# Kernel tuning notes

Measured on AMD Instinct MI355X. Metric: run time of the kernel, lower is better.

## Reference

```python
import jax, jax.numpy as jnp
import numpy as np

B, C, L, D, P = 64, 64, 720, 512, 336
P2, H = P // 2, 512  # H = hidden width of the ProbG branch


def setup_inputs() -> dict:
    key = jax.random.key(0)
    ks = jax.random.split(key, 20)
    def w(k, i, o):
        return jax.random.normal(k, (i, o), jnp.float32) / np.sqrt(i)
    return {
        "x_bsd": jax.random.normal(ks[0], (B, L, C), jnp.float32),
        "z0": jax.random.normal(ks[1], (B, C, D), jnp.float32),
        "y0": jax.random.normal(ks[2], (B, C, P), jnp.float32),
        # ProbG hidden branch (HID_GIVEN_X_V0 -> SS_Z_GIVEN_X_V0)
        "W_h": w(ks[3], L, H),
        "W_ssz": w(ks[4], H, 2 * D),
        # x->z scale/shift flows (versions v2..v5)
        "W_xz_v2": w(ks[5], L, 2 * D),
        "W_xz_v3": w(ks[6], L, 2 * D),
        "W_xz_v4": w(ks[7], L, 2 * D),
        "W_xz_v5": w(ks[8], L, 2 * D),
        # z->x scale/shift flows (v0, v2, v3, v5)
        "W_zx_v0": w(ks[9], D, 2 * L),
        "W_zx_v2": w(ks[10], D, 2 * L),
        "W_zx_v3": w(ks[11], D, 2 * L),
        "W_zx_v5": w(ks[12], D, 2 * L),
        # z->y scale/shift flow (v4, used inside encoding)
        "W_zy_v4": w(ks[13], D, 2 * P),
        # decode heads: ROT_IN_Y_V1 and KOO_Y_GIVEN_Z_V0
        "W_rot": w(ks[14], D, P2),
        "W_koo": w(ks[15], D, 2 * P),
        # Koopman complex params for y-space (a + i b per channel/pair)
        "a_y": jnp.ones((C, P2), jnp.float32),
        "b_y": jnp.zeros((C, P2), jnp.float32) + 0.1,
    }


def _ss(params):
    """Split conditioner output into (positive scale, shift)."""
    s_raw, t = jnp.split(params, 2, axis=-1)
    return jnp.exp(jnp.tanh(s_raw)), t


def _affine(v, cond, W):
    """Scale/shift flow: v <- v * s(cond) + t(cond)."""
    s, t = _ss(jnp.einsum('bck,km->bcm', cond, W))
    return v * s + t


def _rot(u, theta, inv=False):
    """Rotate interleaved (re, im) pairs of u [B,C,P] by angles theta [B,C,P/2]."""
    re, im = u[..., 0::2], u[..., 1::2]
    th = -theta if inv else theta
    c, s = jnp.cos(th), jnp.sin(th)
    return jnp.stack([c * re - s * im, s * re + c * im], axis=-1).reshape(u.shape)


def _koop(u, a, b, inv=False):
    """Koopman unit-complex multiply on interleaved pairs; a,b [C,P/2]."""
    n = jnp.sqrt(a * a + b * b)
    ca, cb = a / n, b / n
    cb = -cb if inv else cb
    re, im = u[..., 0::2], u[..., 1::2]
    return jnp.stack([ca * re - cb * im, cb * re + ca * im], axis=-1).reshape(u.shape)


def reference(x_bsd, z0, y0, W_h, W_ssz, W_xz_v2, W_xz_v3, W_xz_v4, W_xz_v5,
              W_zx_v0, W_zx_v2, W_zx_v3, W_zx_v5, W_zy_v4, W_rot, W_koo, a_y, b_y):
    x = jnp.transpose(x_bsd, (0, 2, 1))  # [B,C,L]
    z = z0 * 0.1                          # [B,C,D]
    y = y0 * 0.1                          # [B,C,P]
    # ---- encoding phase ----
    h = jax.nn.gelu(jnp.einsum('bcl,lk->bck', x, W_h))  # X_to_Z_PROB hidden
    z = _affine(z, h, W_ssz)
    x = _affine(x, z, W_zx_v0)
    z = _affine(z, x, W_xz_v2); x = _affine(x, z, W_zx_v2)
    z = _affine(z, x, W_xz_v3); x = _affine(x, z, W_zx_v3)
    z = _affine(z, x, W_xz_v4); y = _affine(y, z, W_zy_v4)  # Z_to_Y_V4
    z = _affine(z, x, W_xz_v5); x = _affine(x, z, W_zx_v5)
    pre_y = y
    # ---- decode: rotate -> ky -> scale -> ky.inv -> rot.inv -> shift ----
    theta = jnp.pi * jnp.tanh(jnp.einsum('bcd,dp->bcp', z, W_rot))   # [B,C,P/2]
    scale, shift = _ss(jnp.einsum('bcd,dp->bcp', z, W_koo))          # [B,C,P]
    const = _koop(_rot(pre_y, theta), a_y, b_y)
    accu = const * scale
    accu = _rot(_koop(accu, a_y, b_y, inv=True), theta, inv=True) + shift
    return jnp.transpose(accu, (0, 2, 1))  # [B,P,C]
```

## Files before the change

kernel.cpp:

```cpp
#include <hip/hip_runtime.h>
#include <hip/hip_bf16.h>
#include <math.h>

#define BB  64
#define CC  64
#define LL  720
#define LLP 736
#define DD  512
#define PP  336
#define P2C 168
#define HH  512
#define MM  (BB*CC)

typedef _Float16 f16x8 __attribute__((ext_vector_type(8)));
typedef float    f32x4 __attribute__((ext_vector_type(4)));

#define GLDS16(g, l) __builtin_amdgcn_global_load_lds( \
    (const __attribute__((address_space(1))) void*)(g), \
    (__attribute__((address_space(3))) void*)(l), 16, 0, 0)

struct WDesc { const float* src; _Float16* dstHi; _Float16* dstLo;
               int K, N, Kpad, tbase, tilesN; };
struct WTab  { WDesc d[12]; };

__global__ __launch_bounds__(256) void k_convert(WTab tab) {
  __shared__ float tile[16][17];
  const int bid = blockIdx.x;
  int wi = 0;
#pragma unroll
  for (int i = 1; i < 12; ++i) if (bid >= tab.d[i].tbase) wi = i;
  const WDesc d = tab.d[wi];
  const int lt = bid - d.tbase;
  const int tk = lt / d.tilesN, tn = lt % d.tilesN;
  const int k0 = tk * 16, n0 = tn * 16;
  const int tx = threadIdx.x & 15, ty = threadIdx.x >> 4;
  float v = 0.f;
  if (n0 + tx < d.N) v = d.src[(size_t)(k0 + ty) * d.N + n0 + tx];
  tile[ty][tx] = v;
  __syncthreads();
  if (n0 + ty < d.N) {
    const float w = tile[tx][ty];
    const _Float16 h = (_Float16)w;
    const _Float16 l = (_Float16)(w - (float)h);
    const size_t base = (size_t)(n0 + ty) * d.Kpad;
    d.dstHi[base + k0 + tx] = h;
    d.dstLo[base + k0 + tx] = l;
    if (d.Kpad != d.K && k0 + 16 == d.K) {
      d.dstHi[base + d.K + tx] = (_Float16)0.f;
      d.dstLo[base + d.K + tx] = (_Float16)0.f;
    }
  }
}

__global__ __launch_bounds__(256) void k_xpose(const float* __restrict__ xbsd,
                                               _Float16* __restrict__ xhi,
                                               _Float16* __restrict__ xlo) {
  __shared__ float tile[16][17];
  const int b = blockIdx.z, l0 = blockIdx.x * 16, c0 = blockIdx.y * 16;
  const int tx = threadIdx.x, ty = threadIdx.y;
  tile[ty][tx] = xbsd[(size_t)b * LL * CC + (size_t)(l0 + ty) * CC + c0 + tx];
  __syncthreads();
  const float v = tile[tx][ty];
  const _Float16 h = (_Float16)v;
  const _Float16 l = (_Float16)(v - (float)h);
  const size_t m = (size_t)b * CC + c0 + ty;
  xhi[m * LLP + l0 + tx] = h;
  xlo[m * LLP + l0 + tx] = l;
  if (l0 == 704) {
    xhi[m * LLP + 720 + tx] = (_Float16)0.f;
    xlo[m * LLP + 720 + tx] = (_Float16)0.f;
  }
}

template<int EPI, bool DUAL, bool VIN16, bool OUT_T>
__global__ __launch_bounds__(256)
void k_gemm(const _Float16* Ahi, const _Float16* Alo, int lda,
            const _Float16* Whi, const _Float16* Wlo, int ldw,
            const float* Vin32, const _Float16* VinHi,
            const _Float16* VinLo, int ldv, float vscale,
            float* outT32,
            _Float16* outHi, _Float16* outLo, int ldo,
            int Kp, int Nv) {
  constexpr int NB   = DUAL ? 128 : 64;
  constexpr int ABUF = 64 * 32;
  constexpr int BBUF = NB * 32;
  constexpr int SBUF = 2 * ABUF + 2 * BBUF;
  constexpr int NCH  = 8 + 2 * (NB / 16);
  constexpr int NCHW = NCH / 4;
  __shared__ _Float16 smem[2 * SBUF];

  const int m0 = blockIdx.y * 64;
  const int n0 = blockIdx.x * 64;
  const int tid = threadIdx.x;
  const int w = tid >> 6, lane = tid & 63, q = lane >> 4, r = lane & 15;
  const int wr = (w & 1) * 32, wc = (w >> 1) * 32;
  const int lr = lane >> 2, ls = lane & 3;

  f32x4 accS[2][2] = {};
  f32x4 accT[2][2] = {};

  auto stage = [&](int kc, int bsel) {
    const int k0 = kc << 5;
    _Float16* sb = smem + bsel * SBUF;
#pragma unroll
    for (int cc = 0; cc < NCHW; ++cc) {
      const int chunk = w * NCHW + cc;
      const _Float16* gsrc;
      _Float16* ldst;
      if (chunk < 4) {
        const int rb = chunk * 16;
        const int R = rb + lr;
        const int ss = ls ^ ((R >> 1) & 3);
        gsrc = Ahi + (size_t)(m0 + R) * lda + k0 + ss * 8;
        ldst = sb + rb * 32;
      } else if (chunk < 8) {
        const int rb = (chunk - 4) * 16;
        const int R = rb + lr;
        const int ss = ls ^ ((R >> 1) & 3);
        gsrc = Alo + (size_t)(m0 + R) * lda + k0 + ss * 8;
        ldst = sb + ABUF + rb * 32;
      } else if (chunk < 8 + NB / 16) {
        const int rb = (chunk - 8) * 16;
        const int R = rb + lr;
        const int ss = ls ^ ((R >> 1) & 3);
        const int wrow = (R < 64) ? (n0 + R) : (Nv + n0 + (R - 64));
        gsrc = Whi + (size_t)wrow * ldw + k0 + ss * 8;
        ldst = sb + 2 * ABUF + rb * 32;
      } else {
        const int rb = (chunk - 8 - NB / 16) * 16;
        const int R = rb + lr;
        const int ss = ls ^ ((R >> 1) & 3);
        const int wrow = (R < 64) ? (n0 + R) : (Nv + n0 + (R - 64));
        gsrc = Wlo + (size_t)wrow * ldw + k0 + ss * 8;
        ldst = sb + 2 * ABUF + BBUF + rb * 32;
      }
      GLDS16(gsrc, ldst);
    }
  };

  const int nk = Kp >> 5;
  stage(0, 0);
  int cur = 0;
  for (int kc = 0; kc < nk; ++kc) {
    __syncthreads();
    if (kc + 1 < nk) stage(kc + 1, cur ^ 1);
    const _Float16* sb = smem + cur * SBUF;

    f16x8 ah[2], al[2];
#pragma unroll
    for (int rt = 0; rt < 2; ++rt) {
      const int R = wr + rt * 16 + r;
      const int t = (q ^ ((R >> 1) & 3)) * 8;
      ah[rt] = *(const f16x8*)(sb + R * 32 + t);
      al[rt] = *(const f16x8*)(sb + ABUF + R * 32 + t);
    }
#pragma unroll
    for (int ct = 0; ct < 2; ++ct) {
      const int RB = wc + ct * 16 + r;
      const int tb = (q ^ ((RB >> 1) & 3)) * 8;
      const f16x8 bh = *(const f16x8*)(sb + 2 * ABUF + RB * 32 + tb);
      const f16x8 bl = *(const f16x8*)(sb + 2 * ABUF + BBUF + RB * 32 + tb);
#pragma unroll
      for (int rt = 0; rt < 2; ++rt) {
        accS[rt][ct] = __builtin_amdgcn_mfma_f32_16x16x32_f16(ah[rt], bh, accS[rt][ct], 0, 0, 0);
        accS[rt][ct] = __builtin_amdgcn_mfma_f32_16x16x32_f16(al[rt], bh, accS[rt][ct], 0, 0, 0);
        accS[rt][ct] = __builtin_amdgcn_mfma_f32_16x16x32_f16(ah[rt], bl, accS[rt][ct], 0, 0, 0);
      }
      if (DUAL) {
        const int RT = 64 + RB;
        const int tt = (q ^ ((RT >> 1) & 3)) * 8;
        const f16x8 chh = *(const f16x8*)(sb + 2 * ABUF + RT * 32 + tt);
        const f16x8 cll = *(const f16x8*)(sb + 2 * ABUF + BBUF + RT * 32 + tt);
#pragma unroll
        for (int rt = 0; rt < 2; ++rt) {
          accT[rt][ct] = __builtin_amdgcn_mfma_f32_16x16x32_f16(ah[rt], chh, accT[rt][ct], 0, 0, 0);
          accT[rt][ct] = __builtin_amdgcn_mfma_f32_16x16x32_f16(al[rt], chh, accT[rt][ct], 0, 0, 0);
          accT[rt][ct] = __builtin_amdgcn_mfma_f32_16x16x32_f16(ah[rt], cll, accT[rt][ct], 0, 0, 0);
        }
      }
    }
    cur ^= 1;
  }

#pragma unroll
  for (int rt = 0; rt < 2; ++rt) {
    const int mb = m0 + wr + rt * 16 + q * 4;
#pragma unroll
    for (int ct = 0; ct < 2; ++ct) {
      const int n = n0 + wc + ct * 16 + r;
      if (n >= Nv) continue;
      if (EPI == 2) {
        *(f32x4*)(outT32 + (size_t)n * MM + mb) = accS[rt][ct];
      } else if (EPI == 1) {
#pragma unroll
        for (int g = 0; g < 4; ++g) {
          const int m = mb + g;
          const float v = accS[rt][ct][g];
          const float o = 0.5f * v * (1.0f + tanhf(0.7978845608028654f * (v + 0.044715f * v * v * v)));
          const _Float16 h = (_Float16)o;
          outHi[(size_t)m * ldo + n] = h;
          outLo[(size_t)m * ldo + n] = (_Float16)(o - (float)h);
        }
      } else {
        f32x4 o;
#pragma unroll
        for (int g = 0; g < 4; ++g) {
          const int m = mb + g;
          float v;
          if (VIN16) {
            v = (float)VinHi[(size_t)m * ldv + n] + (float)VinLo[(size_t)m * ldv + n];
          } else {
            v = Vin32[(size_t)m * ldv + n];
          }
          const float s = expf(tanhf(accS[rt][ct][g]));
          o[g] = v * vscale * s + accT[rt][ct][g];
        }
        if (OUT_T) {
          *(f32x4*)(outT32 + (size_t)n * MM + mb) = o;
        } else {
#pragma unroll
          for (int g = 0; g < 4; ++g) {
            const int m = mb + g;
            const _Float16 h = (_Float16)o[g];
            outHi[(size_t)m * ldo + n] = h;
            outLo[(size_t)m * ldo + n] = (_Float16)(o[g] - (float)h);
          }
        }
      }
    }
  }
}

__global__ __launch_bounds__(256) void k_final(const float* __restrict__ Pt,
                                               const float* __restrict__ yT,
                                               const float* __restrict__ Ay,
                                               const float* __restrict__ By,
                                               float* __restrict__ out) {
  const int c = threadIdx.x;
  const int j = blockIdx.x * 4 + threadIdx.y;
  const int b = blockIdx.y;
  const int m = b * 64 + c;
  const float th = 3.14159265358979323846f * tanhf(Pt[(size_t)j * MM + m]);
  const float sc0 = expf(tanhf(Pt[(size_t)(168 + 2 * j) * MM + m]));
  const float sc1 = expf(tanhf(Pt[(size_t)(169 + 2 * j) * MM + m]));
  const float t0 = Pt[(size_t)(504 + 2 * j) * MM + m];
  const float t1 = Pt[(size_t)(505 + 2 * j) * MM + m];
  const float re = yT[(size_t)(2 * j) * MM + m];
  const float im = yT[(size_t)(2 * j + 1) * MM + m];
  const float a = Ay[c * P2C + j], bb = By[c * P2C + j];
  const float rn = rsqrtf(a * a + bb * bb);
  const float ca = a * rn, cb = bb * rn;
  float s1v, c1;
  sincosf(th, &s1v, &c1);
  const float r1 = c1 * re - s1v * im, i1 = s1v * re + c1 * im;
  const float r2 = ca * r1 - cb * i1,  i2 = cb * r1 + ca * i1;
  const float r3 = r2 * sc0,           i3 = i2 * sc1;
  const float r4 = ca * r3 + cb * i3,  i4 = ca * i3 - cb * r3;
  const float r5 = c1 * r4 + s1v * i4, i5 = c1 * i4 - s1v * r4;
  out[(size_t)b * PP * CC + (size_t)(2 * j) * CC + c]     = r5 + t0;
  out[(size_t)b * PP * CC + (size_t)(2 * j + 1) * CC + c] = i5 + t1;
}

extern "C" void kernel_launch(void* const* d_in, const int* in_sizes, int n_in,
                              void* d_out, int out_size, void* d_ws, size_t ws_size,
                              hipStream_t stream) {
  const float* x_bsd   = (const float*)d_in[0];
  const float* z0      = (const float*)d_in[1];
  const float* y0      = (const float*)d_in[2];
  const float* W_h     = (const float*)d_in[3];
  const float* W_ssz   = (const float*)d_in[4];
  const float* W_xz_v2 = (const float*)d_in[5];
  const float* W_xz_v3 = (const float*)d_in[6];
  const float* W_xz_v4 = (const float*)d_in[7];
  const float* W_xz_v5 = (const float*)d_in[8];
  const float* W_zx_v0 = (const float*)d_in[9];
  const float* W_zx_v2 = (const float*)d_in[10];
  const float* W_zx_v3 = (const float*)d_in[11];
  const float* W_zy_v4 = (const float*)d_in[13];
  const float* W_rot   = (const float*)d_in[14];
  const float* W_koo   = (const float*)d_in[15];
  const float* a_y     = (const float*)d_in[16];
  const float* b_y     = (const float*)d_in[17];
  float* out = (float*)d_out;

  char* p = (char*)d_ws;
  auto alloc = [&](size_t bytes) -> void* {
    void* r = (void*)p; p += (bytes + 255) & ~(size_t)255; return r;
  };
  float*    yT  = (float*)alloc((size_t)PP * MM * 4);
  float*    Pt  = (float*)alloc((size_t)(P2C * 5) * MM * 4);
  _Float16* xhi = (_Float16*)alloc((size_t)MM * LLP * 2);
  _Float16* xlo = (_Float16*)alloc((size_t)MM * LLP * 2);
  _Float16* zhi = (_Float16*)alloc((size_t)MM * DD * 2);
  _Float16* zlo = (_Float16*)alloc((size_t)MM * DD * 2);
  _Float16* hhi = (_Float16*)alloc((size_t)MM * HH * 2);
  _Float16* hlo = (_Float16*)alloc((size_t)MM * HH * 2);
  auto wpair = [&](size_t elems, _Float16** lo) -> _Float16* {
    _Float16* hi = (_Float16*)alloc(elems * 2);
    *lo = (_Float16*)alloc(elems * 2);
    return hi;
  };
  _Float16 *tWhL, *tWsszL, *tWxz2L, *tWxz3L, *tWxz4L, *tWxz5L;
  _Float16 *tWzx0L, *tWzx2L, *tWzx3L, *tWzyL, *tWcatL;
  _Float16* tWh   = wpair((size_t)HH * LLP, &tWhL);
  _Float16* tWssz = wpair((size_t)(2*DD) * DD, &tWsszL);
  _Float16* tWxz2 = wpair((size_t)(2*DD) * LLP, &tWxz2L);
  _Float16* tWxz3 = wpair((size_t)(2*DD) * LLP, &tWxz3L);
  _Float16* tWxz4 = wpair((size_t)(2*DD) * LLP, &tWxz4L);
  _Float16* tWxz5 = wpair((size_t)(2*DD) * LLP, &tWxz5L);
  _Float16* tWzx0 = wpair((size_t)1536 * DD, &tWzx0L);
  _Float16* tWzx2 = wpair((size_t)1536 * DD, &tWzx2L);
  _Float16* tWzx3 = wpair((size_t)1536 * DD, &tWzx3L);
  _Float16* tWzy  = wpair((size_t)768 * DD, &tWzyL);
  _Float16* tWcat = wpair((size_t)896 * DD, &tWcatL);

  WTab tab;
  int base = 0;
  auto put = [&](int i, const float* src, _Float16* dh, _Float16* dl,
                 int K, int N, int Kpad) {
    const int tN = (N + 15) / 16;
    tab.d[i] = WDesc{src, dh, dl, K, N, Kpad, base, tN};
    base += ((K + 15) / 16) * tN;
  };
  put(0,  W_h,     tWh,   tWhL,   LL, HH,   LLP);
  put(1,  W_ssz,   tWssz, tWsszL, DD, 2*DD, DD);
  put(2,  W_xz_v2, tWxz2, tWxz2L, LL, 2*DD, LLP);
  put(3,  W_xz_v3, tWxz3, tWxz3L, LL, 2*DD, LLP);
  put(4,  W_xz_v4, tWxz4, tWxz4L, LL, 2*DD, LLP);
  put(5,  W_xz_v5, tWxz5, tWxz5L, LL, 2*DD, LLP);
  put(6,  W_zx_v0, tWzx0, tWzx0L, DD, 2*LL, DD);
  put(7,  W_zx_v2, tWzx2, tWzx2L, DD, 2*LL, DD);
  put(8,  W_zx_v3, tWzx3, tWzx3L, DD, 2*LL, DD);
  put(9,  W_zy_v4, tWzy,  tWzyL,  DD, 2*PP, DD);
  put(10, W_rot,   tWcat, tWcatL, DD, P2C,  DD);
  put(11, W_koo,   tWcat + (size_t)P2C * DD, tWcatL + (size_t)P2C * DD, DD, 2*PP, DD);
  const int total_tiles = base;

  k_convert<<<dim3(total_tiles), dim3(256), 0, stream>>>(tab);
  k_xpose<<<dim3(45, 4, 64), dim3(16, 16), 0, stream>>>(x_bsd, xhi, xlo);

  const dim3 blk(256);
  k_gemm<1, false, false, false><<<dim3(8, 64), blk, 0, stream>>>(
      xhi, xlo, LLP, tWh, tWhL, LLP,
      nullptr, nullptr, nullptr, 0, 0.f, nullptr, hhi, hlo, HH, LLP, HH);
  k_gemm<0, true, false, false><<<dim3(8, 64), blk, 0, stream>>>(
      hhi, hlo, HH, tWssz, tWsszL, DD,
      z0, nullptr, nullptr, DD, 0.1f, nullptr, zhi, zlo, DD, DD, DD);
  k_gemm<0, true, true, false><<<dim3(12, 64), blk, 0, stream>>>(
      zhi, zlo, DD, tWzx0, tWzx0L, DD,
      nullptr, xhi, xlo, LLP, 1.f, nullptr, xhi, xlo, LLP, DD, LL);
  k_gemm<0, true, true, false><<<dim3(8, 64), blk, 0, stream>>>(
      xhi, xlo, LLP, tWxz2, tWxz2L, LLP,
      nullptr, zhi, zlo, DD, 1.f, nullptr, zhi, zlo, DD, LLP, DD);
  k_gemm<0, true, true, false><<<dim3(12, 64), blk, 0, stream>>>(
      zhi, zlo, DD, tWzx2, tWzx2L, DD,
      nullptr, xhi, xlo, LLP, 1.f, nullptr, xhi, xlo, LLP, DD, LL);
  k_gemm<0, true, true, false><<<dim3(8, 64), blk, 0, stream>>>(
      xhi, xlo, LLP, tWxz3, tWxz3L, LLP,
      nullptr, zhi, zlo, DD, 1.f, nullptr, zhi, zlo, DD, LLP, DD);
  k_gemm<0, true, true, false><<<dim3(12, 64), blk, 0, stream>>>(
      zhi, zlo, DD, tWzx3, tWzx3L, DD,
      nullptr, xhi, xlo, LLP, 1.f, nullptr, xhi, xlo, LLP, DD, LL);
  k_gemm<0, true, true, false><<<dim3(8, 64), blk, 0, stream>>>(
      xhi, xlo, LLP, tWxz4, tWxz4L, LLP,
      nullptr, zhi, zlo, DD, 1.f, nullptr, zhi, zlo, DD, LLP, DD);
  k_gemm<0, true, false, true><<<dim3(6, 64), blk, 0, stream>>>(
      zhi, zlo, DD, tWzy, tWzyL, DD,
      y0, nullptr, nullptr, PP, 0.1f, yT, nullptr, nullptr, 0, DD, PP);
  k_gemm<0, true, true, false><<<dim3(8, 64), blk, 0, stream>>>(
      xhi, xlo, LLP, tWxz5, tWxz5L, LLP,
      nullptr, zhi, zlo, DD, 1.f, nullptr, zhi, zlo, DD, LLP, DD);
  k_gemm<2, false, false, true><<<dim3(14, 64), blk, 0, stream>>>(
      zhi, zlo, DD, tWcat, tWcatL, DD,
      nullptr, nullptr, nullptr, 0, 0.f, Pt, nullptr, nullptr, 0, DD, P2C * 5);
  k_final<<<dim3(42, 64), dim3(64, 4), 0, stream>>>(Pt, yT, a_y, b_y, out);
}
```

Measured before the change: 457.6 us.

## Load A fragments directly from global into registers, staging only W in LDS

The A operand (hi/lo f16 activations) is no longer staged through shared memory. Each wave reads its MFMA fragments straight from global memory into registers, with one-step register prefetch. LDS staging is kept only for the weight tiles, which shrinks shared memory and cuts LDS traffic. In exchange, A rows are read by both column-waves (duplicated global/L2 traffic), and global latency lands on the MFMA path with only a single prefetch stage.

```diff
diff --git a/kernel.cpp b/kernel.cpp
--- a/kernel.cpp
+++ b/kernel.cpp
@@ -82,10 +82,9 @@
             _Float16* outHi, _Float16* outLo, int ldo,
             int Kp, int Nv) {
   constexpr int NB   = DUAL ? 128 : 64;
-  constexpr int ABUF = 64 * 32;
   constexpr int BBUF = NB * 32;
-  constexpr int SBUF = 2 * ABUF + 2 * BBUF;
-  constexpr int NCH  = 8 + 2 * (NB / 16);
+  constexpr int SBUF = 2 * BBUF;
+  constexpr int NCH  = 2 * (NB / 16);
   constexpr int NCHW = NCH / 4;
   __shared__ _Float16 smem[2 * SBUF];
 
@@ -107,78 +106,76 @@
       const int chunk = w * NCHW + cc;
       const _Float16* gsrc;
       _Float16* ldst;
-      if (chunk < 4) {
+      if (chunk < NB / 16) {
         const int rb = chunk * 16;
-        const int R = rb + lr;
-        const int ss = ls ^ ((R >> 1) & 3);
-        gsrc = Ahi + (size_t)(m0 + R) * lda + k0 + ss * 8;
-        ldst = sb + rb * 32;
-      } else if (chunk < 8) {
-        const int rb = (chunk - 4) * 16;
-        const int R = rb + lr;
-        const int ss = ls ^ ((R >> 1) & 3);
-        gsrc = Alo + (size_t)(m0 + R) * lda + k0 + ss * 8;
-        ldst = sb + ABUF + rb * 32;
-      } else if (chunk < 8 + NB / 16) {
-        const int rb = (chunk - 8) * 16;
         const int R = rb + lr;
         const int ss = ls ^ ((R >> 1) & 3);
         const int wrow = (R < 64) ? (n0 + R) : (Nv + n0 + (R - 64));
         gsrc = Whi + (size_t)wrow * ldw + k0 + ss * 8;
-        ldst = sb + 2 * ABUF + rb * 32;
+        ldst = sb + rb * 32;
       } else {
-        const int rb = (chunk - 8 - NB / 16) * 16;
+        const int rb = (chunk - NB / 16) * 16;
         const int R = rb + lr;
         const int ss = ls ^ ((R >> 1) & 3);
         const int wrow = (R < 64) ? (n0 + R) : (Nv + n0 + (R - 64));
         gsrc = Wlo + (size_t)wrow * ldw + k0 + ss * 8;
-        ldst = sb + 2 * ABUF + BBUF + rb * 32;
+        ldst = sb + BBUF + rb * 32;
       }
       GLDS16(gsrc, ldst);
     }
   };
 
+  const _Float16* aH0 = Ahi + (size_t)(m0 + wr + r)      * lda + q * 8;
+  const _Float16* aH1 = Ahi + (size_t)(m0 + wr + 16 + r) * lda + q * 8;
+  const _Float16* aL0 = Alo + (size_t)(m0 + wr + r)      * lda + q * 8;
+  const _Float16* aL1 = Alo + (size_t)(m0 + wr + 16 + r) * lda + q * 8;
+
   const int nk = Kp >> 5;
   stage(0, 0);
+  f16x8 c0h = *(const f16x8*)(aH0);
+  f16x8 c1h = *(const f16x8*)(aH1);
+  f16x8 c0l = *(const f16x8*)(aL0);
+  f16x8 c1l = *(const f16x8*)(aL1);
+  f16x8 p0h = c0h, p1h = c1h, p0l = c0l, p1l = c1l;
   int cur = 0;
   for (int kc = 0; kc < nk; ++kc) {
     __syncthreads();
-    if (kc + 1 < nk) stage(kc + 1, cur ^ 1);
+    if (kc + 1 < nk) {
+      stage(kc + 1, cur ^ 1);
+      const int ko = (kc + 1) << 5;
+      p0h = *(const f16x8*)(aH0 + ko);
+      p1h = *(const f16x8*)(aH1 + ko);
+      p0l = *(const f16x8*)(aL0 + ko);
+      p1l = *(const f16x8*)(aL1 + ko);
+    }
     const _Float16* sb = smem + cur * SBUF;
 
-    f16x8 ah[2], al[2];
-#pragma unroll
-    for (int rt = 0; rt < 2; ++rt) {
-      const int R = wr + rt * 16 + r;
-      const int t = (q ^ ((R >> 1) & 3)) * 8;
-      ah[rt] = *(const f16x8*)(sb + R * 32 + t);
-      al[rt] = *(const f16x8*)(sb + ABUF + R * 32 + t);
-    }
 #pragma unroll
     for (int ct = 0; ct < 2; ++ct) {
       const int RB = wc + ct * 16 + r;
       const int tb = (q ^ ((RB >> 1) & 3)) * 8;
-      const f16x8 bh = *(const f16x8*)(sb + 2 * ABUF + RB * 32 + tb);
-      const f16x8 bl = *(const f16x8*)(sb + 2 * ABUF + BBUF + RB * 32 + tb);
-#pragma unroll
-      for (int rt = 0; rt < 2; ++rt) {
-        accS[rt][ct] = __builtin_amdgcn_mfma_f32_16x16x32_f16(ah[rt], bh, accS[rt][ct], 0, 0, 0);
-        accS[rt][ct] = __builtin_amdgcn_mfma_f32_16x16x32_f16(al[rt], bh, accS[rt][ct], 0, 0, 0);
-        accS[rt][ct] = __builtin_amdgcn_mfma_f32_16x16x32_f16(ah[rt], bl, accS[rt][ct], 0, 0, 0);
-      }
+      const f16x8 bh = *(const f16x8*)(sb + RB * 32 + tb);
+      const f16x8 bl = *(const f16x8*)(sb + BBUF + RB * 32 + tb);
+      accS[0][ct] = __builtin_amdgcn_mfma_f32_16x16x32_f16(c0h, bh, accS[0][ct], 0, 0, 0);
+      accS[0][ct] = __builtin_amdgcn_mfma_f32_16x16x32_f16(c0l, bh, accS[0][ct], 0, 0, 0);
+      accS[0][ct] = __builtin_amdgcn_mfma_f32_16x16x32_f16(c0h, bl, accS[0][ct], 0, 0, 0);
+      accS[1][ct] = __builtin_amdgcn_mfma_f32_16x16x32_f16(c1h, bh, accS[1][ct], 0, 0, 0);
+      accS[1][ct] = __builtin_amdgcn_mfma_f32_16x16x32_f16(c1l, bh, accS[1][ct], 0, 0, 0);
+      accS[1][ct] = __builtin_amdgcn_mfma_f32_16x16x32_f16(c1h, bl, accS[1][ct], 0, 0, 0);
       if (DUAL) {
         const int RT = 64 + RB;
         const int tt = (q ^ ((RT >> 1) & 3)) * 8;
-        const f16x8 chh = *(const f16x8*)(sb + 2 * ABUF + RT * 32 + tt);
-        const f16x8 cll = *(const f16x8*)(sb + 2 * ABUF + BBUF + RT * 32 + tt);
-#pragma unroll
-        for (int rt = 0; rt < 2; ++rt) {
-          accT[rt][ct] = __builtin_amdgcn_mfma_f32_16x16x32_f16(ah[rt], chh, accT[rt][ct], 0, 0, 0);
-          accT[rt][ct] = __builtin_amdgcn_mfma_f32_16x16x32_f16(al[rt], chh, accT[rt][ct], 0, 0, 0);
-          accT[rt][ct] = __builtin_amdgcn_mfma_f32_16x16x32_f16(ah[rt], cll, accT[rt][ct], 0, 0, 0);
-        }
+        const f16x8 chh = *(const f16x8*)(sb + RT * 32 + tt);
+        const f16x8 cll = *(const f16x8*)(sb + BBUF + RT * 32 + tt);
+        accT[0][ct] = __builtin_amdgcn_mfma_f32_16x16x32_f16(c0h, chh, accT[0][ct], 0, 0, 0);
+        accT[0][ct] = __builtin_amdgcn_mfma_f32_16x16x32_f16(c0l, chh, accT[0][ct], 0, 0, 0);
+        accT[0][ct] = __builtin_amdgcn_mfma_f32_16x16x32_f16(c0h, cll, accT[0][ct], 0, 0, 0);
+        accT[1][ct] = __builtin_amdgcn_mfma_f32_16x16x32_f16(c1h, chh, accT[1][ct], 0, 0, 0);
+        accT[1][ct] = __builtin_amdgcn_mfma_f32_16x16x32_f16(c1l, chh, accT[1][ct], 0, 0, 0);
+        accT[1][ct] = __builtin_amdgcn_mfma_f32_16x16x32_f16(c1h, cll, accT[1][ct], 0, 0, 0);
       }
     }
+    c0h = p0h; c1h = p1h; c0l = p0l; c1l = p1l;
     cur ^= 1;
   }
 
```

Result: slower. 514.9 us (+12.5%).
